# Kernel optimization log

Hardware: AMD Instinct MI355X
Metric: run time of the kernel (lower is better)

The kernel has to match this reference:

```python
import jax, jax.numpy as jnp
import numpy as np

H = 64        # gru_hiddens
HEADS = 4     # n_heads
HID = 64      # n_hidden (is_concat=False -> out_features)
RT = 4        # role_types
APT = 3       # agents per type
N_AMB = 1023  # ambiguous agents; N = 1 + N_AMB = 1024
SLOPE = 0.2


def _leaky(x):
    return jnp.where(x >= 0, x, SLOPE * x)


def _linear(x, W, b):
    return x @ W.T + b


def setup_inputs() -> dict:
    key = jax.random.key(0)
    ks = jax.random.split(key, 18)
    s = 0.1
    return {
        "hidden": jax.random.normal(ks[0], (1, H), jnp.float32),
        "ambiguous": jax.random.normal(ks[1], (N_AMB, H), jnp.float32),
        "type_agents": jax.random.normal(ks[2], (RT, APT, 1, H), jnp.float32),
        # per-role-type routing MLPs and merge/self MLPs
        "W_self": jax.random.normal(ks[3], (H, H), jnp.float32) * s,
        "b_self": jnp.zeros((H,), jnp.float32),
        "W_merge": jax.random.normal(ks[4], (H, 2 * H), jnp.float32) * s,
        "b_merge": jnp.zeros((H,), jnp.float32),
        "W_trans": jax.random.normal(ks[5], (RT, H, H), jnp.float32) * s,
        "b_trans": jnp.zeros((RT, H), jnp.float32),
        # GATv2 params (no biases)
        "W_l": jax.random.normal(ks[6], (HEADS * HID, H), jnp.float32) * s,
        "W_r": jax.random.normal(ks[7], (HEADS * HID, H), jnp.float32) * s,
        "w_attn": jax.random.normal(ks[8], (HID,), jnp.float32) * s,
        # type_define MLP: 2H -> 64 -> 128 -> RT
        "Wd0": jax.random.normal(ks[9], (64, 2 * H), jnp.float32) * s,
        "bd0": jnp.zeros((64,), jnp.float32),
        "Wd1": jax.random.normal(ks[10], (128, 64), jnp.float32) * s,
        "bd1": jnp.zeros((128,), jnp.float32),
        "Wd2": jax.random.normal(ks[11], (RT, 128), jnp.float32) * s,
        "bd2": jnp.zeros((RT,), jnp.float32),
    }


def reference(hidden, ambiguous, type_agents,
              W_self, b_self, W_merge, b_merge, W_trans, b_trans,
              W_l, W_r, w_attn,
              Wd0, bd0, Wd1, bd1, Wd2, bd2):
    # per-role-type routing + merge
    hidden_1 = _linear(hidden, W_self, b_self)  # [1, H]
    for t in range(RT):
        # mean over agents of trans_mlp[t](agent)
        tmp = (jnp.einsum('aih,oh->aio', type_agents[t], W_trans[t]) + b_trans[t]).mean(axis=0)
        hidden_1 = _leaky(_linear(jnp.concatenate([hidden_1, tmp], axis=-1), W_merge, b_merge))

    h = jnp.concatenate([hidden_1, ambiguous], axis=0)  # [N, H], N = 1 + N_AMB
    n = h.shape[0]

    # GATv2 dense pairwise attention (adjacency all-True; dropout in eval = identity)
    g_l = (h @ W_l.T).reshape(n, HEADS, HID)
    g_r = (h @ W_r.T).reshape(n, HEADS, HID)
    # g_sum[i, j] = g_l[j] + g_r[i]  -> [N, N, HEADS, HID]
    g_sum = g_l[None, :, :, :] + g_r[:, None, :, :]
    e = jnp.einsum('ijhf,f->ijh', _leaky(g_sum), w_attn)  # [N, N, HEADS]
    a = jax.nn.softmax(e, axis=1)
    attn_res = jnp.einsum('ijh,jhf->ihf', a, g_r)  # [N, HEADS, HID]
    gat_out = attn_res.mean(axis=1)  # is_concat=False -> mean over heads, [N, HID]

    hidden_2 = gat_out[0]  # [HID]
    rep = jnp.broadcast_to(hidden_2[None, :], (ambiguous.shape[0], HID))
    x = jnp.concatenate([ambiguous, rep], axis=-1)  # [N_AMB, 2H]
    x = _leaky(_linear(x, Wd0, bd0))
    x = _leaky(_linear(x, Wd1, bd1))
    x = _linear(x, Wd2, bd2)
    return jax.nn.sigmoid(x)  # [N_AMB, RT]
```

## Files before the change

kernel.cpp:

```cpp
#include <hip/hip_runtime.h>
#include <math.h>

#define SLOPE 0.2f

__device__ __forceinline__ float leaky(float x) { return x >= 0.f ? x : SLOPE * x; }


#define POISON_U32 0xAAAAAAAAu

__global__ __launch_bounds__(256) void k_fused(
    const float* __restrict__ hidden, const float* __restrict__ ambiguous,
    const float* __restrict__ type_agents,
    const float* __restrict__ W_self, const float* __restrict__ b_self,
    const float* __restrict__ W_merge, const float* __restrict__ b_merge,
    const float* __restrict__ W_trans, const float* __restrict__ b_trans,
    const float* __restrict__ W_l, const float* __restrict__ W_r,
    const float* __restrict__ w_attn,
    const float* __restrict__ Wd0, const float* __restrict__ bd0,
    const float* __restrict__ Wd1, const float* __restrict__ bd1,
    const float* __restrict__ Wd2, const float* __restrict__ bd2,
    float* __restrict__ ws, float* __restrict__ out)
{
    __shared__ __align__(16) float sh[128];
    __shared__ __align__(16) float tm[64];
    __shared__ __align__(16) float h1[64];
    __shared__ __align__(16) float hrow[4][64];
    __shared__ __align__(16) float x[4][128];
    __shared__ __align__(16) float y0[4][64];
    __shared__ __align__(16) float y1[4][128];

    const int t = threadIdx.x;
    const int o = t & 63;
    const int r = t >> 6;
    const bool lead = (t < 64);

    {
        int row = blockIdx.x * 4 + r;
        x[r][o] = (row < 1023) ? ambiguous[row * 64 + o] : 0.f;
    }

    float hv = 0.f;
    if (lead) {
        float acc = b_self[o];
        const float4* w4 = (const float4*)(W_self + o * 64);
#pragma unroll
        for (int k = 0; k < 16; k++) {
            float4 w = w4[k];
            acc += w.x * hidden[k*4+0] + w.y * hidden[k*4+1]
                 + w.z * hidden[k*4+2] + w.w * hidden[k*4+3];
        }
        hv = acc;
    }
    for (int tt = 0; tt < 4; tt++) {
        if (lead) {
            sh[o] = hv;
            tm[o] = (type_agents[tt*192 + o] + type_agents[tt*192 + 64 + o]
                   + type_agents[tt*192 + 128 + o]) * (1.f / 3.f);
        }
        __syncthreads();
        if (lead) {
            float tv = b_trans[tt*64 + o];
            const float4* w4 = (const float4*)(W_trans + tt*4096 + o*64);
#pragma unroll
            for (int k = 0; k < 16; k++) {
                float4 w = w4[k];
                tv += w.x * tm[k*4+0] + w.y * tm[k*4+1]
                    + w.z * tm[k*4+2] + w.w * tm[k*4+3];
            }
            sh[64 + o] = tv;
        }
        __syncthreads();
        if (lead) {
            float acc = b_merge[o];
            const float4* w4 = (const float4*)(W_merge + o * 128);
#pragma unroll
            for (int k = 0; k < 32; k++) {
                float4 w = w4[k];
                acc += w.x * sh[k*4+0] + w.y * sh[k*4+1]
                     + w.z * sh[k*4+2] + w.w * sh[k*4+3];
            }
            hv = leaky(acc);
        }
        __syncthreads();
    }
    if (lead) h1[o] = hv;

    float4 wl[16], wr[16];
    {
        const float4* Wl4 = (const float4*)(W_l + t * 64);
        const float4* Wr4 = (const float4*)(W_r + t * 64);
#pragma unroll
        for (int k = 0; k < 16; k++) { wl[k] = Wl4[k]; wr[k] = Wr4[k]; }
    }
    __syncthreads();

    float g0 = 0.f;
#pragma unroll
    for (int k = 0; k < 16; k++) {
        float4 w = wr[k];
        g0 += w.x * h1[k*4+0] + w.y * h1[k*4+1] + w.z * h1[k*4+2] + w.w * h1[k*4+3];
    }

    {
        int j = blockIdx.x * 4 + r;
        hrow[r][o] = (j == 0) ? h1[o] : ambiguous[(j - 1) * 64 + o];
    }
    __syncthreads();

    float accl[4] = {0.f, 0.f, 0.f, 0.f};
    float accr[4] = {0.f, 0.f, 0.f, 0.f};
#pragma unroll
    for (int kk = 0; kk < 16; kk++) {
        float4 a = wl[kk], b = wr[kk];
#pragma unroll
        for (int rr = 0; rr < 4; rr++) {
            float x0 = hrow[rr][kk*4+0], x1 = hrow[rr][kk*4+1];
            float x2 = hrow[rr][kk*4+2], x3 = hrow[rr][kk*4+3];
            accl[rr] += a.x*x0 + a.y*x1 + a.z*x2 + a.w*x3;
            accr[rr] += b.x*x0 + b.y*x1 + b.z*x2 + b.w*x3;
        }
    }

    const int head = r;
    const float wa = w_attn[o];
    float numsum = 0.f, denp = 0.f;
#pragma unroll
    for (int rr = 0; rr < 4; rr++) {
        float ec = leaky(accl[rr] + g0) * wa;
#pragma unroll
        for (int off = 32; off; off >>= 1) ec += __shfl_xor(ec, off, 64);
        float w = expf(ec);
        numsum += w * accr[rr];
        denp   += w;
    }
    atomicAdd(&ws[t], numsum);
    if (o == 0) atomicAdd(&ws[256 + head], denp);

    unsigned* wsu = (unsigned*)ws;
    __syncthreads();
    if (t == 0) {
        __threadfence();
        atomicAdd(&wsu[260], 1u);
        while (__hip_atomic_load(&wsu[260], __ATOMIC_RELAXED,
                                 __HIP_MEMORY_SCOPE_AGENT) != POISON_U32 + 256u) {
            __builtin_amdgcn_s_sleep(1);
        }
        __threadfence();
    }
    __syncthreads();

    if (t < 64) {
        float s = 0.f;
#pragma unroll
        for (int h = 0; h < 4; h++) {
            float nm = __hip_atomic_load(&ws[h*64 + t], __ATOMIC_RELAXED,
                                         __HIP_MEMORY_SCOPE_AGENT);
            float dn = __hip_atomic_load(&ws[256 + h], __ATOMIC_RELAXED,
                                         __HIP_MEMORY_SCOPE_AGENT);
            s += nm / dn;
        }
        float h2 = 0.25f * s;
        x[0][64 + t] = h2; x[1][64 + t] = h2; x[2][64 + t] = h2; x[3][64 + t] = h2;
    }
    __syncthreads();

    {
        float acc = bd0[o];
        const float4* w4 = (const float4*)(Wd0 + o * 128);
        const float4* xr = (const float4*)(&x[r][0]);
#pragma unroll
        for (int kk = 0; kk < 32; kk++) {
            float4 w = w4[kk]; float4 xv = xr[kk];
            acc += w.x*xv.x + w.y*xv.y + w.z*xv.z + w.w*xv.w;
        }
        y0[r][o] = leaky(acc);
    }
    __syncthreads();

#pragma unroll
    for (int rep = 0; rep < 2; rep++) {
        int idx = rep * 256 + t;
        int rr = idx >> 7, oo = idx & 127;
        float acc = bd1[oo];
        const float4* w4 = (const float4*)(Wd1 + oo * 64);
        const float4* yr = (const float4*)(&y0[rr][0]);
#pragma unroll
        for (int kk = 0; kk < 16; kk++) {
            float4 w = w4[kk]; float4 yv = yr[kk];
            acc += w.x*yv.x + w.y*yv.y + w.z*yv.z + w.w*yv.w;
        }
        y1[rr][oo] = leaky(acc);
    }
    __syncthreads();

    if (t < 16) {
        int rr = t >> 2, c = t & 3;
        int row = blockIdx.x * 4 + rr;
        if (row < 1023) {
            float acc = bd2[c];
            const float4* w4 = (const float4*)(Wd2 + c * 128);
            const float4* yr = (const float4*)(&y1[rr][0]);
#pragma unroll
            for (int kk = 0; kk < 32; kk++) {
                float4 w = w4[kk]; float4 yv = yr[kk];
                acc += w.x*yv.x + w.y*yv.y + w.z*yv.z + w.w*yv.w;
            }
            out[row * 4 + c] = 1.f / (1.f + expf(-acc));
        }
    }
}

extern "C" void kernel_launch(void* const* d_in, const int* in_sizes, int n_in,
                              void* d_out, int out_size, void* d_ws, size_t ws_size,
                              hipStream_t stream)
{
    const float* hidden      = (const float*)d_in[0];
    const float* ambiguous   = (const float*)d_in[1];
    const float* type_agents = (const float*)d_in[2];
    const float* W_self      = (const float*)d_in[3];
    const float* b_self      = (const float*)d_in[4];
    const float* W_merge     = (const float*)d_in[5];
    const float* b_merge     = (const float*)d_in[6];
    const float* W_trans     = (const float*)d_in[7];
    const float* b_trans     = (const float*)d_in[8];
    const float* W_l         = (const float*)d_in[9];
    const float* W_r         = (const float*)d_in[10];
    const float* w_attn      = (const float*)d_in[11];
    const float* Wd0         = (const float*)d_in[12];
    const float* bd0         = (const float*)d_in[13];
    const float* Wd1         = (const float*)d_in[14];
    const float* bd1         = (const float*)d_in[15];
    const float* Wd2         = (const float*)d_in[16];
    const float* bd2         = (const float*)d_in[17];
    float* ws  = (float*)d_ws;
    float* out = (float*)d_out;

    k_fused<<<256, 256, 0, stream>>>(hidden, ambiguous, type_agents,
                                     W_self, b_self, W_merge, b_merge,
                                     W_trans, b_trans, W_l, W_r, w_attn,
                                     Wd0, bd0, Wd1, bd1, Wd2, bd2, ws, out);
}
```

Baseline: 133.8 us.

## Shrink grid to 64 blocks with per-block partials instead of atomics

Cuts the grid from 256 to 64 blocks, each handling 16 rows. Each block writes its attention numerator and denominator partials to its own workspace slot instead of issuing float atomics, and after the grid barrier every block reduces all 64 slots. The first wave runs the serial routing MLP while the other waves load rows, using block-level fences in place of __syncthreads. W_l is streamed from memory rather than held in registers. The goal is to cut atomic contention and grid-barrier cost. In exchange it adds more per-thread work, more registers for the 16-row accumulators, and a redundant 64-slot reduction in every block.

```diff
diff --git a/kernel.cpp b/kernel.cpp
--- a/kernel.cpp
+++ b/kernel.cpp
@@ -2,11 +2,12 @@
 #include <math.h>
 
 #define SLOPE 0.2f
+#define NBLK 64
+#define PART_STRIDE 320
+#define CNT_IDX (NBLK * PART_STRIDE)
+#define POISON_U32 0xAAAAAAAAu
 
 __device__ __forceinline__ float leaky(float x) { return x >= 0.f ? x : SLOPE * x; }
-
-
-#define POISON_U32 0xAAAAAAAAu
 
 __global__ __launch_bounds__(256) void k_fused(
     const float* __restrict__ hidden, const float* __restrict__ ambiguous,
@@ -24,53 +25,65 @@
     __shared__ __align__(16) float sh[128];
     __shared__ __align__(16) float tm[64];
     __shared__ __align__(16) float h1[64];
-    __shared__ __align__(16) float hrow[4][64];
-    __shared__ __align__(16) float x[4][128];
-    __shared__ __align__(16) float y0[4][64];
-    __shared__ __align__(16) float y1[4][128];
+    __shared__ __align__(16) float hrow[16][64];
+    __shared__ __align__(16) float hs[4][64];
+    __shared__ __align__(16) float x[16][128];
+    __shared__ __align__(16) float y0[16][64];
+    __shared__ __align__(16) float y1[16][128];
 
     const int t = threadIdx.x;
     const int o = t & 63;
     const int r = t >> 6;
-    const bool lead = (t < 64);
-
+    const int b = blockIdx.x;
+
+    float4 wr[16];
     {
-        int row = blockIdx.x * 4 + r;
-        x[r][o] = (row < 1023) ? ambiguous[row * 64 + o] : 0.f;
-    }
-
-    float hv = 0.f;
-    if (lead) {
-        float acc = b_self[o];
-        const float4* w4 = (const float4*)(W_self + o * 64);
-#pragma unroll
-        for (int k = 0; k < 16; k++) {
-            float4 w = w4[k];
-            acc += w.x * hidden[k*4+0] + w.y * hidden[k*4+1]
-                 + w.z * hidden[k*4+2] + w.w * hidden[k*4+3];
-        }
-        hv = acc;
-    }
-    for (int tt = 0; tt < 4; tt++) {
-        if (lead) {
+        const float4* Wr4 = (const float4*)(W_r + t * 64);
+#pragma unroll
+        for (int k = 0; k < 16; k++) wr[k] = Wr4[k];
+    }
+
+    if (r != 0) {
+        int u = t - 64;
+#pragma unroll
+        for (int i = 0; i < 6; i++) {
+            int idx = u + 192 * i;
+            if (idx < 1024) {
+                int rl = idx >> 6, c = idx & 63;
+                int j = b * 16 + rl;
+                hrow[rl][c] = (j == 0) ? 0.f : ambiguous[(j - 1) * 64 + c];
+            }
+        }
+    } else {
+        float hv;
+        {
+            float acc = b_self[o];
+            const float4* w4 = (const float4*)(W_self + o * 64);
+#pragma unroll
+            for (int k = 0; k < 16; k++) {
+                float4 w = w4[k];
+                acc += w.x * hidden[k*4+0] + w.y * hidden[k*4+1]
+                     + w.z * hidden[k*4+2] + w.w * hidden[k*4+3];
+            }
+            hv = acc;
+        }
+        for (int tt = 0; tt < 4; tt++) {
             sh[o] = hv;
             tm[o] = (type_agents[tt*192 + o] + type_agents[tt*192 + 64 + o]
                    + type_agents[tt*192 + 128 + o]) * (1.f / 3.f);
-        }
-        __syncthreads();
-        if (lead) {
+            __threadfence_block();
             float tv = b_trans[tt*64 + o];
-            const float4* w4 = (const float4*)(W_trans + tt*4096 + o*64);
-#pragma unroll
-            for (int k = 0; k < 16; k++) {
-                float4 w = w4[k];
-                tv += w.x * tm[k*4+0] + w.y * tm[k*4+1]
-                    + w.z * tm[k*4+2] + w.w * tm[k*4+3];
+            {
+                const float4* w4 = (const float4*)(W_trans + tt*4096 + o*64);
+#pragma unroll
+                for (int k = 0; k < 16; k++) {
+                    float4 w = w4[k];
+                    tv += w.x * tm[k*4+0] + w.y * tm[k*4+1]
+                        + w.z * tm[k*4+2] + w.w * tm[k*4+3];
+                }
             }
             sh[64 + o] = tv;
-        }
-        __syncthreads();
-        if (lead) {
+            __threadfence_block();
             float acc = b_merge[o];
             const float4* w4 = (const float4*)(W_merge + o * 128);
 #pragma unroll
@@ -80,19 +93,12 @@
                      + w.z * sh[k*4+2] + w.w * sh[k*4+3];
             }
             hv = leaky(acc);
-        }
-        __syncthreads();
-    }
-    if (lead) h1[o] = hv;
-
-    float4 wl[16], wr[16];
-    {
-        const float4* Wl4 = (const float4*)(W_l + t * 64);
-        const float4* Wr4 = (const float4*)(W_r + t * 64);
-#pragma unroll
-        for (int k = 0; k < 16; k++) { wl[k] = Wl4[k]; wr[k] = Wr4[k]; }
-    }
-    __syncthreads();
+            __threadfence_block();
+        }
+        h1[o] = hv;
+    }
+    __syncthreads();
+    if (b == 0 && t < 64) hrow[0][o] = h1[o];
 
     float g0 = 0.f;
 #pragma unroll
@@ -100,32 +106,31 @@
         float4 w = wr[k];
         g0 += w.x * h1[k*4+0] + w.y * h1[k*4+1] + w.z * h1[k*4+2] + w.w * h1[k*4+3];
     }
-
+    __syncthreads();
+
+    float accl[16], accr[16];
+#pragma unroll
+    for (int rr = 0; rr < 16; rr++) { accl[rr] = 0.f; accr[rr] = 0.f; }
     {
-        int j = blockIdx.x * 4 + r;
-        hrow[r][o] = (j == 0) ? h1[o] : ambiguous[(j - 1) * 64 + o];
-    }
-    __syncthreads();
-
-    float accl[4] = {0.f, 0.f, 0.f, 0.f};
-    float accr[4] = {0.f, 0.f, 0.f, 0.f};
-#pragma unroll
-    for (int kk = 0; kk < 16; kk++) {
-        float4 a = wl[kk], b = wr[kk];
-#pragma unroll
-        for (int rr = 0; rr < 4; rr++) {
-            float x0 = hrow[rr][kk*4+0], x1 = hrow[rr][kk*4+1];
-            float x2 = hrow[rr][kk*4+2], x3 = hrow[rr][kk*4+3];
-            accl[rr] += a.x*x0 + a.y*x1 + a.z*x2 + a.w*x3;
-            accr[rr] += b.x*x0 + b.y*x1 + b.z*x2 + b.w*x3;
-        }
-    }
-
-    const int head = r;
+        const float4* Wl4 = (const float4*)(W_l + t * 64);
+#pragma unroll
+        for (int kk = 0; kk < 16; kk++) {
+            float4 a = Wl4[kk];
+            float4 c = wr[kk];
+#pragma unroll
+            for (int rr = 0; rr < 16; rr++) {
+                float x0 = hrow[rr][kk*4+0], x1 = hrow[rr][kk*4+1];
+                float x2 = hrow[rr][kk*4+2], x3 = hrow[rr][kk*4+3];
+                accl[rr] += a.x*x0 + a.y*x1 + a.z*x2 + a.w*x3;
+                accr[rr] += c.x*x0 + c.y*x1 + c.z*x2 + c.w*x3;
+            }
+        }
+    }
+
     const float wa = w_attn[o];
     float numsum = 0.f, denp = 0.f;
 #pragma unroll
-    for (int rr = 0; rr < 4; rr++) {
+    for (int rr = 0; rr < 16; rr++) {
         float ec = leaky(accl[rr] + g0) * wa;
 #pragma unroll
         for (int off = 32; off; off >>= 1) ec += __shfl_xor(ec, off, 64);
@@ -133,73 +138,83 @@
         numsum += w * accr[rr];
         denp   += w;
     }
-    atomicAdd(&ws[t], numsum);
-    if (o == 0) atomicAdd(&ws[256 + head], denp);
+    ws[b * PART_STRIDE + t] = numsum;
+    if (o == 0) ws[b * PART_STRIDE + 256 + r] = denp;
 
     unsigned* wsu = (unsigned*)ws;
     __syncthreads();
     if (t == 0) {
         __threadfence();
-        atomicAdd(&wsu[260], 1u);
-        while (__hip_atomic_load(&wsu[260], __ATOMIC_RELAXED,
-                                 __HIP_MEMORY_SCOPE_AGENT) != POISON_U32 + 256u) {
+        atomicAdd(&wsu[CNT_IDX], 1u);
+        while (__hip_atomic_load(&wsu[CNT_IDX], __ATOMIC_RELAXED,
+                                 __HIP_MEMORY_SCOPE_AGENT) != POISON_U32 + NBLK) {
             __builtin_amdgcn_s_sleep(1);
         }
         __threadfence();
     }
     __syncthreads();
 
+#pragma unroll
+    for (int i = 0; i < 4; i++) {
+        int idx = t + 256 * i;
+        int rl = idx >> 6, c = idx & 63;
+        int row = b * 16 + rl;
+        x[rl][c] = (row < 1023) ? ambiguous[row * 64 + c] : 0.f;
+    }
+    float nsum = 0.f;
+#pragma unroll 8
+    for (int bb = 0; bb < NBLK; bb++) nsum += ws[bb * PART_STRIDE + t];
+    float d = ws[o * PART_STRIDE + 256 + r];
+#pragma unroll
+    for (int off = 32; off; off >>= 1) d += __shfl_xor(d, off, 64);
+    hs[r][o] = nsum / d;
+    __syncthreads();
     if (t < 64) {
-        float s = 0.f;
-#pragma unroll
-        for (int h = 0; h < 4; h++) {
-            float nm = __hip_atomic_load(&ws[h*64 + t], __ATOMIC_RELAXED,
-                                         __HIP_MEMORY_SCOPE_AGENT);
-            float dn = __hip_atomic_load(&ws[256 + h], __ATOMIC_RELAXED,
-                                         __HIP_MEMORY_SCOPE_AGENT);
-            s += nm / dn;
-        }
-        float h2 = 0.25f * s;
-        x[0][64 + t] = h2; x[1][64 + t] = h2; x[2][64 + t] = h2; x[3][64 + t] = h2;
-    }
-    __syncthreads();
-
-    {
-        float acc = bd0[o];
-        const float4* w4 = (const float4*)(Wd0 + o * 128);
-        const float4* xr = (const float4*)(&x[r][0]);
+        float h2 = 0.25f * (hs[0][o] + hs[1][o] + hs[2][o] + hs[3][o]);
+#pragma unroll
+        for (int rl = 0; rl < 16; rl++) x[rl][64 + o] = h2;
+    }
+    __syncthreads();
+
+#pragma unroll
+    for (int i = 0; i < 4; i++) {
+        int idx = t + 256 * i;
+        int rl = idx >> 6, c = idx & 63;
+        float acc = bd0[c];
+        const float4* w4 = (const float4*)(Wd0 + c * 128);
+        const float4* xr = (const float4*)(&x[rl][0]);
 #pragma unroll
         for (int kk = 0; kk < 32; kk++) {
             float4 w = w4[kk]; float4 xv = xr[kk];
             acc += w.x*xv.x + w.y*xv.y + w.z*xv.z + w.w*xv.w;
         }
-        y0[r][o] = leaky(acc);
-    }
-    __syncthreads();
-
-#pragma unroll
-    for (int rep = 0; rep < 2; rep++) {
-        int idx = rep * 256 + t;
-        int rr = idx >> 7, oo = idx & 127;
-        float acc = bd1[oo];
-        const float4* w4 = (const float4*)(Wd1 + oo * 64);
-        const float4* yr = (const float4*)(&y0[rr][0]);
+        y0[rl][c] = leaky(acc);
+    }
+    __syncthreads();
+
+#pragma unroll
+    for (int i = 0; i < 8; i++) {
+        int idx = t + 256 * i;
+        int rl = idx >> 7, c = idx & 127;
+        float acc = bd1[c];
+        const float4* w4 = (const float4*)(Wd1 + c * 64);
+        const float4* yr = (const float4*)(&y0[rl][0]);
 #pragma unroll
         for (int kk = 0; kk < 16; kk++) {
             float4 w = w4[kk]; float4 yv = yr[kk];
             acc += w.x*yv.x + w.y*yv.y + w.z*yv.z + w.w*yv.w;
         }
-        y1[rr][oo] = leaky(acc);
-    }
-    __syncthreads();
-
-    if (t < 16) {
-        int rr = t >> 2, c = t & 3;
-        int row = blockIdx.x * 4 + rr;
+        y1[rl][c] = leaky(acc);
+    }
+    __syncthreads();
+
+    if (t < 64) {
+        int rl = t >> 2, c = t & 3;
+        int row = b * 16 + rl;
         if (row < 1023) {
             float acc = bd2[c];
             const float4* w4 = (const float4*)(Wd2 + c * 128);
-            const float4* yr = (const float4*)(&y1[rr][0]);
+            const float4* yr = (const float4*)(&y1[rl][0]);
 #pragma unroll
             for (int kk = 0; kk < 32; kk++) {
                 float4 w = w4[kk]; float4 yv = yr[kk];
@@ -235,8 +250,8 @@
     float* ws  = (float*)d_ws;
     float* out = (float*)d_out;
 
-    k_fused<<<256, 256, 0, stream>>>(hidden, ambiguous, type_agents,
-                                     W_self, b_self, W_merge, b_merge,
-                                     W_trans, b_trans, W_l, W_r, w_attn,
-                                     Wd0, bd0, Wd1, bd1, Wd2, bd2, ws, out);
+    k_fused<<<NBLK, 256, 0, stream>>>(hidden, ambiguous, type_agents,
+                                      W_self, b_self, W_merge, b_merge,
+                                      W_trans, b_trans, W_l, W_r, w_attn,
+                                      Wd0, bd0, Wd1, bd1, Wd2, bd2, ws, out);
 }
```

Result: slower. 158.8 us (+18.7%).
